# Kernel tuning notes

Measured on AMD Instinct MI355X. Metric: run time of the kernel, lower is better.

## Reference

```python
import jax, jax.numpy as jnp
import numpy as np

V, E, IN, OUT, K, NREL = 50000, 640000, 128, 128, 4, 237
D = IN // K   # 32
OD = OUT // K # 32

def setup_inputs() -> dict:
    key = jax.random.key(0)
    ks = jax.random.split(key, 20)
    s = 0.05
    return {
        'node_repr': jax.random.normal(ks[0], (V, IN), jnp.float32),
        'rel_repr': jax.random.normal(ks[1], (2 * NREL, IN), jnp.float32),
        'src': jax.random.randint(ks[2], (E,), 0, V, jnp.int32),
        'dst': jax.random.randint(ks[3], (E,), 0, V, jnp.int32),
        'etype': jax.random.randint(ks[4], (E,), 0, 2 * NREL, jnp.int32),
        'norm': jax.random.uniform(ks[5], (E,), jnp.float32),
        'node_w': jax.random.normal(ks[6], (K, IN, D), jnp.float32) * s,
        'node_rel_w': jax.random.normal(ks[7], (K, IN, D), jnp.float32) * s,
        'in_w': jax.random.normal(ks[8], (K, D, OD), jnp.float32) * s,
        'out_w': jax.random.normal(ks[9], (K, D, OD), jnp.float32) * s,
        'att_w': jax.random.normal(ks[10], (2 * D, 1), jnp.float32) * s,
        'loop_rel': jax.random.normal(ks[11], (1, IN), jnp.float32) * s,
        'loop_w': jax.random.normal(ks[12], (IN, OUT), jnp.float32) * s,
        'w_rel': jax.random.normal(ks[13], (IN, OUT), jnp.float32) * s,
        'bias': jnp.zeros((OUT,), jnp.float32),
        'bn_gamma': jnp.ones((OUT,), jnp.float32),
        'bn_beta': jnp.zeros((OUT,), jnp.float32),
    }

def reference(node_repr, rel_repr, src, dst, etype, norm,
              node_w, node_rel_w, in_w, out_w, att_w,
              loop_rel, loop_w, w_rel, bias, bn_gamma, bn_beta):
    e = E
    half = e // 2
    rel = rel_repr  # no bases
    # per-edge composition (opn='mult'): src feature * relation feature
    edge_comp = node_repr[src] * rel[etype]                      # [E, IN]
    edge_data = jnp.einsum('ei,kid->ekd', edge_comp, node_rel_w)  # [E, K, D]
    node_data = jnp.einsum('ei,kid->ekd', node_repr[dst], node_w) # [E, K, D]
    cat = jnp.concatenate([edge_data, node_data], axis=-1)       # [E, K, 2D]
    att = jax.nn.relu(cat @ att_w)                               # [E, K, 1]
    att = jax.nn.softmax(att, axis=1)                            # softmax over K factors
    edge_data = edge_data * att                                  # broadcast over D
    # factorized projection: first half edges -> in_w, second half -> out_w
    msg_in = jnp.einsum('ekd,kdo->eko', edge_data[:half], in_w)
    msg_out = jnp.einsum('ekd,kdo->eko', edge_data[half:], out_w)
    msg = jnp.concatenate([msg_in, msg_out], axis=0).reshape(e, OUT)
    msg = msg * norm[:, None]
    # scatter-sum into destination nodes, then /3 (drop_rate=0)
    h = jax.ops.segment_sum(msg, dst, num_segments=V) / 3.0      # [V, OUT]
    # self-loop term
    h = h + ((h * loop_rel) @ loop_w) / 3.0
    h = h + bias
    # BatchNorm1d (training-mode batch stats, biased variance, eps=1e-5)
    mean = jnp.mean(h, axis=0)
    var = jnp.var(h, axis=0)
    h = bn_gamma * (h - mean) * jax.lax.rsqrt(var + 1e-5) + bn_beta
    node_out = jnp.tanh(h)
    rel_out = rel @ w_rel
    return node_out, rel_out
```

## Files before the change

### kernel.cpp

```cpp
#include <hip/hip_runtime.h>

namespace {
constexpr int V = 50000;
constexpr int E = 640000;
constexpr int HALF = 320000;
constexpr int NREL2 = 474;
constexpr int C = 128;
constexpr int NCHUNK = (V + 255) / 256;
}

typedef _Float16 h4 __attribute__((ext_vector_type(4)));
typedef _Float16 f16x8 __attribute__((ext_vector_type(8)));
typedef float f32x4 __attribute__((ext_vector_type(4)));

__global__ void prep_kernel(const float* __restrict__ nrw, const float* __restrict__ nw,
                            const float* __restrict__ inw, const float* __restrict__ outw,
                            const float* __restrict__ aw,
                            float* __restrict__ cbuf, float* __restrict__ bbuf,
                            float* __restrict__ Min, float* __restrict__ Mout) {
  int tid = blockIdx.x * 256 + threadIdx.x;
  if (tid < 512) {
    int k = tid >> 7, i = tid & 127;
    float acc = 0.f;
    for (int d = 0; d < 32; ++d) acc += nrw[k*4096 + i*32 + d] * aw[d];
    cbuf[tid] = acc;
  } else if (tid < 1024) {
    int u = tid - 512; int k = u >> 7, i = u & 127;
    float acc = 0.f;
    for (int d = 0; d < 32; ++d) acc += nw[k*4096 + i*32 + d] * aw[32 + d];
    bbuf[u] = acc;
  } else if (tid < 1024 + 16384) {
    int u = tid - 1024; int k = u >> 12, rem = u & 4095, i = rem >> 5, o = rem & 31;
    float acc = 0.f;
    for (int d = 0; d < 32; ++d) acc += nrw[k*4096 + i*32 + d] * inw[k*1024 + d*32 + o];
    Min[u] = acc;
  } else if (tid < 1024 + 32768) {
    int u = tid - 1024 - 16384; int k = u >> 12, rem = u & 4095, i = rem >> 5, o = rem & 31;
    float acc = 0.f;
    for (int d = 0; d < 32; ++d) acc += nrw[k*4096 + i*32 + d] * outw[k*1024 + d*32 + o];
    Mout[u] = acc;
  }
}

__global__ void mh_kernel(const float* __restrict__ Min, const float* __restrict__ Mout,
                          _Float16* __restrict__ Mh) {
  int u = blockIdx.x * 256 + threadIdx.x;
  int i = u & 127;
  int o16 = (u >> 7) & 15;
  int ot = (u >> 11) & 1;
  int kk = (u >> 12) & 3;
  int d = (u >> 14) & 1;
  int o = ot * 16 + o16;
  float v = (d ? Mout : Min)[kk * 4096 + i * 32 + o];
  Mh[u] = (_Float16)v;
}

__global__ __launch_bounds__(256) void cast_kernel(const float* __restrict__ src,
                                                   _Float16* __restrict__ dst, int n8) {
  int u = blockIdx.x * 256 + threadIdx.x;
  if (u >= n8) return;
  const float4 v0 = *(const float4*)(src + (size_t)u * 8);
  const float4 v1 = *(const float4*)(src + (size_t)u * 8 + 4);
  f16x8 o;
  o[0] = (_Float16)v0.x; o[1] = (_Float16)v0.y;
  o[2] = (_Float16)v0.z; o[3] = (_Float16)v0.w;
  o[4] = (_Float16)v1.x; o[5] = (_Float16)v1.y;
  o[6] = (_Float16)v1.z; o[7] = (_Float16)v1.w;
  *(f16x8*)(dst + (size_t)u * 8) = o;
}

__global__ __launch_bounds__(256) void qnode_kernel(const float* __restrict__ nrp,
                                                    const float* __restrict__ bbuf,
                                                    float* __restrict__ qbuf) {
  const int t = blockIdx.x * 16 + (threadIdx.x >> 4);
  const int l = threadIdx.x & 15;
  if (t >= V) return;
  const float* row = nrp + (size_t)t * C + l * 8;
  float4 a0 = *(const float4*)(row);
  float4 a1 = *(const float4*)(row + 4);
  float p[4];
#pragma unroll
  for (int k = 0; k < 4; ++k) {
    const float* brow = bbuf + k * C + l * 8;
    float4 b0 = *(const float4*)(brow);
    float4 b1 = *(const float4*)(brow + 4);
    p[k] = a0.x * b0.x + a0.y * b0.y + a0.z * b0.z + a0.w * b0.w
         + a1.x * b1.x + a1.y * b1.y + a1.z * b1.z + a1.w * b1.w;
  }
#pragma unroll
  for (int m = 1; m < 16; m <<= 1) {
#pragma unroll
    for (int k = 0; k < 4; ++k) p[k] += __shfl_xor(p[k], m);
  }
  if (l == 0) *(float4*)(qbuf + 4 * (size_t)t) = make_float4(p[0], p[1], p[2], p[3]);
}

__global__ void hist_kernel(const int* __restrict__ dst, int* __restrict__ cnt,
                            int* __restrict__ cin) {
  int e = blockIdx.x * 256 + threadIdx.x;
  if (e < E) {
    int t = dst[e];
    atomicAdd(&cnt[t], 1);
    if (e < HALF) atomicAdd(&cin[t], 1);
  }
}

__global__ void scan_sum_kernel(const int* __restrict__ cnt, int* __restrict__ bsum) {
  __shared__ int sd[256];
  int tid = threadIdx.x;
  int idx = blockIdx.x * 256 + tid;
  int v = (idx < V) ? cnt[idx] : 0;
  sd[tid] = v; __syncthreads();
  for (int s = 128; s > 0; s >>= 1) {
    if (tid < s) sd[tid] += sd[tid + s];
    __syncthreads();
  }
  if (tid == 0) bsum[blockIdx.x] = sd[0];
}

__global__ void scan_top_kernel(int* __restrict__ bsum) {
  __shared__ int sd[256];
  int tid = threadIdx.x;
  int v = (tid < NCHUNK) ? bsum[tid] : 0;
  sd[tid] = v; __syncthreads();
  for (int ofs = 1; ofs < 256; ofs <<= 1) {
    int t = (tid >= ofs) ? sd[tid - ofs] : 0;
    __syncthreads();
    sd[tid] += t;
    __syncthreads();
  }
  if (tid < NCHUNK) bsum[tid] = sd[tid] - v;
}

__global__ void scan_apply_kernel(const int* __restrict__ cnt, const int* __restrict__ cin,
                                  const int* __restrict__ bsum, int4* __restrict__ ninfo) {
  __shared__ int sd[256];
  int tid = threadIdx.x;
  int idx = blockIdx.x * 256 + tid;
  int v = (idx < V) ? cnt[idx] : 0;
  sd[tid] = v; __syncthreads();
  for (int ofs = 1; ofs < 256; ofs <<= 1) {
    int t = (tid >= ofs) ? sd[tid - ofs] : 0;
    __syncthreads();
    sd[tid] += t;
    __syncthreads();
  }
  if (idx < V) {
    int off = bsum[blockIdx.x] + sd[tid] - v;
    ninfo[idx] = make_int4(off, v, cin[idx], 0);
  }
}

__global__ void place_kernel(const int* __restrict__ dst, const int* __restrict__ src,
                             const int* __restrict__ etype, const float* __restrict__ norm,
                             const int4* __restrict__ ninfo,
                             int* __restrict__ cur_in, int* __restrict__ cur_out,
                             int2* __restrict__ em) {
  int e = blockIdx.x * 256 + threadIdx.x;
  if (e < E) {
    int t = dst[e];
    int off = ninfo[t].x;
    int pos;
    if (e < HALF) {
      pos = off + atomicAdd(&cur_in[t], 1);
    } else {
      pos = off + ninfo[t].z + atomicAdd(&cur_out[t], 1);
    }
    em[pos] = make_int2(src[e] | (etype[e] << 16), __float_as_int(norm[e]));
  }
}

__global__ __launch_bounds__(256) void fused_kernel(
    const _Float16* __restrict__ nrp_h, const _Float16* __restrict__ rel_h,
    const int4* __restrict__ ninfo, const float* __restrict__ qbuf,
    const float* __restrict__ cbuf, const int2* __restrict__ em,
    const _Float16* __restrict__ Mh, float* __restrict__ h) {
  __shared__ __align__(16) _Float16 z16[16384];
  const int w = threadIdx.x >> 6;
  const int lane = threadIdx.x & 63;
  const int dirg = lane >> 5;
  const int slot = (lane >> 4) & 1;
  const int ll = lane & 15;
  const int ch0 = ll * 8;

  float4 ckA[4], ckB[4];
#pragma unroll
  for (int k = 0; k < 4; ++k) {
    ckA[k] = *(const float4*)(cbuf + k * C + ch0);
    ckB[k] = *(const float4*)(cbuf + k * C + ch0 + 4);
  }

  for (int nn = 0; nn < 4; ++nn) {
    const int node = w * 4 + nn;
    const int t = blockIdx.x * 16 + node;
    const int4 nfo = ninfo[t];
    const int start = nfo.x, deg = nfo.y, ni = nfo.z;
    const float4 q4 = *(const float4*)(qbuf + 4 * (size_t)t);
    const int sidx = dirg ? ni : 0;
    const int nmy = dirg ? (deg - ni) : ni;
    const int nmax = max(ni, deg - ni);

    float4 zA[4], zB[4];
#pragma unroll
    for (int k = 0; k < 4; ++k) {
      zA[k] = make_float4(0.f, 0.f, 0.f, 0.f);
      zB[k] = make_float4(0.f, 0.f, 0.f, 0.f);
    }

    if (nmax > 0) {
      int2 em0 = em[start + min(sidx + slot, deg - 1)];
      int2 em1 = em[start + min(sidx + 2 + slot, deg - 1)];
      f16x8 ah = *(const f16x8*)(nrp_h + (size_t)(em0.x & 0xFFFF) * C + ch0);
      f16x8 bh = *(const f16x8*)(rel_h + (size_t)((em0.x >> 16) & 0x1FF) * C + ch0);

      for (int j = 0; j < nmax; j += 2) {
        int2 em2 = em1;
        if (j + 4 < nmax) em2 = em[start + min(sidx + j + 4 + slot, deg - 1)];
        f16x8 ahn = ah, bhn = bh;
        if (j + 2 < nmax) {
          ahn = *(const f16x8*)(nrp_h + (size_t)(em1.x & 0xFFFF) * C + ch0);
          bhn = *(const f16x8*)(rel_h + (size_t)((em1.x >> 16) & 0x1FF) * C + ch0);
        }
        float4 xA, xB;
        xA.x = (float)ah[0] * (float)bh[0];
        xA.y = (float)ah[1] * (float)bh[1];
        xA.z = (float)ah[2] * (float)bh[2];
        xA.w = (float)ah[3] * (float)bh[3];
        xB.x = (float)ah[4] * (float)bh[4];
        xB.y = (float)ah[5] * (float)bh[5];
        xB.z = (float)ah[6] * (float)bh[6];
        xB.w = (float)ah[7] * (float)bh[7];
        float p0 = xA.x * ckA[0].x + xA.y * ckA[0].y + xA.z * ckA[0].z + xA.w * ckA[0].w
                 + xB.x * ckB[0].x + xB.y * ckB[0].y + xB.z * ckB[0].z + xB.w * ckB[0].w;
        float p1 = xA.x * ckA[1].x + xA.y * ckA[1].y + xA.z * ckA[1].z + xA.w * ckA[1].w
                 + xB.x * ckB[1].x + xB.y * ckB[1].y + xB.z * ckB[1].z + xB.w * ckB[1].w;
        float p2 = xA.x * ckA[2].x + xA.y * ckA[2].y + xA.z * ckA[2].z + xA.w * ckA[2].w
                 + xB.x * ckB[2].x + xB.y * ckB[2].y + xB.z * ckB[2].z + xB.w * ckB[2].w;
        float p3 = xA.x * ckA[3].x + xA.y * ckA[3].y + xA.z * ckA[3].z + xA.w * ckA[3].w
                 + xB.x * ckB[3].x + xB.y * ckB[3].y + xB.z * ckB[3].z + xB.w * ckB[3].w;
#pragma unroll
        for (int m = 1; m < 16; m <<= 1) {
          p0 += __shfl_xor(p0, m);
          p1 += __shfl_xor(p1, m);
          p2 += __shfl_xor(p2, m);
          p3 += __shfl_xor(p3, m);
        }
        float l0 = fmaxf(p0 + q4.x, 0.f);
        float l1 = fmaxf(p1 + q4.y, 0.f);
        float l2 = fmaxf(p2 + q4.z, 0.f);
        float l3 = fmaxf(p3 + q4.w, 0.f);
        float e0f = __expf(l0), e1f = __expf(l1);
        float e2f = __expf(l2), e3f = __expf(l3);
        float nr = __int_as_float(em0.y);
        float inv = ((j + slot) < nmy) ? (nr / (e0f + e1f + e2f + e3f)) : 0.f;
        float w0 = e0f * inv, w1 = e1f * inv, w2 = e2f * inv, w3 = e3f * inv;
        zA[0].x += w0 * xA.x; zA[0].y += w0 * xA.y; zA[0].z += w0 * xA.z; zA[0].w += w0 * xA.w;
        zB[0].x += w0 * xB.x; zB[0].y += w0 * xB.y; zB[0].z += w0 * xB.z; zB[0].w += w0 * xB.w;
        zA[1].x += w1 * xA.x; zA[1].y += w1 * xA.y; zA[1].z += w1 * xA.z; zA[1].w += w1 * xA.w;
        zB[1].x += w1 * xB.x; zB[1].y += w1 * xB.y; zB[1].z += w1 * xB.z; zB[1].w += w1 * xB.w;
        zA[2].x += w2 * xA.x; zA[2].y += w2 * xA.y; zA[2].z += w2 * xA.z; zA[2].w += w2 * xA.w;
        zB[2].x += w2 * xB.x; zB[2].y += w2 * xB.y; zB[2].z += w2 * xB.z; zB[2].w += w2 * xB.w;
        zA[3].x += w3 * xA.x; zA[3].y += w3 * xA.y; zA[3].z += w3 * xA.z; zA[3].w += w3 * xA.w;
        zB[3].x += w3 * xB.x; zB[3].y += w3 * xB.y; zB[3].z += w3 * xB.z; zB[3].w += w3 * xB.w;
        em0 = em1; em1 = em2;
        ah = ahn; bh = bhn;
      }
    }

#pragma unroll
    for (int k = 0; k < 4; ++k) {
      zA[k].x += __shfl_xor(zA[k].x, 16);
      zA[k].y += __shfl_xor(zA[k].y, 16);
      zA[k].z += __shfl_xor(zA[k].z, 16);
      zA[k].w += __shfl_xor(zA[k].w, 16);
      zB[k].x += __shfl_xor(zB[k].x, 16);
      zB[k].y += __shfl_xor(zB[k].y, 16);
      zB[k].z += __shfl_xor(zB[k].z, 16);
      zB[k].w += __shfl_xor(zB[k].w, 16);
    }
    if (slot == 0) {
      const int swz = (node & 7) << 4;
      char* zb = (char*)z16 + node * 2048 + dirg * 1024 + ((ll * 16) ^ swz);
#pragma unroll
      for (int k = 0; k < 4; ++k) {
        f16x8 o;
        o[0] = (_Float16)zA[k].x; o[1] = (_Float16)zA[k].y;
        o[2] = (_Float16)zA[k].z; o[3] = (_Float16)zA[k].w;
        o[4] = (_Float16)zB[k].x; o[5] = (_Float16)zB[k].y;
        o[6] = (_Float16)zB[k].z; o[7] = (_Float16)zB[k].w;
        *(f16x8*)(zb + k * 256) = o;
      }
    }
  }
  __syncthreads();

  const int kk = w;
  const int lo16 = lane & 15;
  const int kq = lane >> 4;
  {
    const int anode = lo16;
    const int aswz = (anode & 7) << 4;
    const char* zb = (const char*)z16 + anode * 2048 + kk * 256;
    f16x8 a[2][4];
#pragma unroll
    for (int d = 0; d < 2; ++d)
#pragma unroll
      for (int kc = 0; kc < 4; ++kc)
        a[d][kc] = *(const f16x8*)(zb + d * 1024 + ((kc * 64 + kq * 16) ^ aswz));

    f32x4 c0 = {0.f, 0.f, 0.f, 0.f};
    f32x4 c1 = {0.f, 0.f, 0.f, 0.f};
#pragma unroll
    for (int d = 0; d < 2; ++d)
#pragma unroll
      for (int kc = 0; kc < 4; ++kc) {
        const _Float16* mb = Mh + (((d * 4 + kk) * 2) * 16 + lo16) * 128 + kc * 32 + kq * 8;
        f16x8 b0 = *(const f16x8*)(mb);
        f16x8 b1 = *(const f16x8*)(mb + 2048);
        c0 = __builtin_amdgcn_mfma_f32_16x16x32_f16(a[d][kc], b0, c0, 0, 0, 0);
        c1 = __builtin_amdgcn_mfma_f32_16x16x32_f16(a[d][kc], b1, c1, 0, 0, 0);
      }

    const float third = 1.f / 3.f;
#pragma unroll
    for (int r = 0; r < 4; ++r) {
      int tt = blockIdx.x * 16 + kq * 4 + r;
      if (tt < V) {
        size_t hb = (size_t)tt * C + kk * 32 + lo16;
        h[hb] = c0[r] * third;
        h[hb + 16] = c1[r] * third;
      }
    }
  }
}

__global__ __launch_bounds__(256, 4) void selfloop_kernel(
    float* __restrict__ h, const float* __restrict__ lr,
    const float* __restrict__ lw, const float* __restrict__ bias,
    float* __restrict__ bnsum, float* __restrict__ bnsq) {
  __shared__ float xr[4][8][128];
  __shared__ float red[256];
  const int tid = threadIdx.x;
  const int w = tid >> 6, lane = tid & 63;

  const int c0 = 2 * lane, c1 = c0 + 1;
  const float lr0 = lr[c0], lr1 = lr[c1];
  const float bv0 = bias[c0], bv1 = bias[c1];
  float s0 = 0.f, s1 = 0.f, sq0 = 0.f, sq1 = 0.f;

  const int wg = blockIdx.x * 4 + w;
  const int nw = gridDim.x * 4;
  for (int rb = wg * 8; rb < V; rb += nw * 8) {
    const int nrows = min(8, V - rb);
    float2 hv[8];
#pragma unroll
    for (int rr = 0; rr < 8; ++rr) {
      if (rr < nrows) {
        hv[rr] = *(const float2*)(h + (size_t)(rb + rr) * C + c0);
      } else {
        hv[rr] = make_float2(0.f, 0.f);
      }
      xr[w][rr][c0] = hv[rr].x * lr0;
      xr[w][rr][c1] = hv[rr].y * lr1;
    }
    float acc[8][2] = {};
    for (int i = 0; i < C; ++i) {
      float2 lwv = *(const float2*)(lw + i * C + c0);
#pragma unroll
      for (int rr = 0; rr < 8; ++rr) {
        float xv = xr[w][rr][i];
        acc[rr][0] += xv * lwv.x;
        acc[rr][1] += xv * lwv.y;
      }
    }
    const float third = 1.f / 3.f;
#pragma unroll
    for (int rr = 0; rr < 8; ++rr) {
      if (rr < nrows) {
        float h0 = hv[rr].x + acc[rr][0] * third + bv0;
        float h1 = hv[rr].y + acc[rr][1] * third + bv1;
        *(float2*)(h + (size_t)(rb + rr) * C + c0) = make_float2(h0, h1);
        s0 += h0; s1 += h1; sq0 += h0 * h0; sq1 += h1 * h1;
      }
    }
  }

  __syncthreads();
  red[tid] = s0; __syncthreads();
  if (tid < 64) {
    float v = red[tid] + red[tid + 64] + red[tid + 128] + red[tid + 192];
    atomicAdd(&bnsum[2 * tid], v);
  }
  __syncthreads();
  red[tid] = s1; __syncthreads();
  if (tid < 64) {
    float v = red[tid] + red[tid + 64] + red[tid + 128] + red[tid + 192];
    atomicAdd(&bnsum[2 * tid + 1], v);
  }
  __syncthreads();
  red[tid] = sq0; __syncthreads();
  if (tid < 64) {
    float v = red[tid] + red[tid + 64] + red[tid + 128] + red[tid + 192];
    atomicAdd(&bnsq[2 * tid], v);
  }
  __syncthreads();
  red[tid] = sq1; __syncthreads();
  if (tid < 64) {
    float v = red[tid] + red[tid + 64] + red[tid + 128] + red[tid + 192];
    atomicAdd(&bnsq[2 * tid + 1], v);
  }
}

__global__ void tanh_kernel(float* __restrict__ h,
                            const float* __restrict__ bnsum, const float* __restrict__ bnsq,
                            const float* __restrict__ gamma, const float* __restrict__ beta) {
  int idx = blockIdx.x * 256 + threadIdx.x;
  int base = idx * 4;
  if (base >= V * C) return;
  int j = base & 127;
  const float invV = 1.f / (float)V;
  float4 v = *(float4*)(h + base);
  float o[4] = {v.x, v.y, v.z, v.w};
#pragma unroll
  for (int cidx = 0; cidx < 4; ++cidx) {
    float mean = bnsum[j + cidx] * invV;
    float var = bnsq[j + cidx] * invV - mean * mean;
    float sc = gamma[j + cidx] * rsqrtf(var + 1e-5f);
    float sh = beta[j + cidx] - sc * mean;
    o[cidx] = tanhf(sc * o[cidx] + sh);
  }
  v.x = o[0]; v.y = o[1]; v.z = o[2]; v.w = o[3];
  *(float4*)(h + base) = v;
}

__global__ __launch_bounds__(128) void relout_kernel(
    const float* __restrict__ rel, const float* __restrict__ wrel,
    float* __restrict__ out) {
  __shared__ float rr[128];
  int tid = threadIdx.x;
  int row = blockIdx.x;
  rr[tid] = rel[row * C + tid];
  __syncthreads();
  float acc = 0.f;
#pragma unroll 4
  for (int i = 0; i < C; ++i) acc += rr[i] * wrel[i * C + tid];
  out[row * C + tid] = acc;
}

extern "C" void kernel_launch(void* const* d_in, const int* in_sizes, int n_in,
                              void* d_out, int out_size, void* d_ws, size_t ws_size,
                              hipStream_t stream) {
  const float* node_repr  = (const float*)d_in[0];
  const float* rel_repr   = (const float*)d_in[1];
  const int*   src        = (const int*)d_in[2];
  const int*   dst        = (const int*)d_in[3];
  const int*   etype      = (const int*)d_in[4];
  const float* norm       = (const float*)d_in[5];
  const float* node_w     = (const float*)d_in[6];
  const float* node_rel_w = (const float*)d_in[7];
  const float* in_w       = (const float*)d_in[8];
  const float* out_w      = (const float*)d_in[9];
  const float* att_w      = (const float*)d_in[10];
  const float* loop_rel   = (const float*)d_in[11];
  const float* loop_w     = (const float*)d_in[12];
  const float* w_rel      = (const float*)d_in[13];
  const float* bias       = (const float*)d_in[14];
  const float* bn_gamma   = (const float*)d_in[15];
  const float* bn_beta    = (const float*)d_in[16];

  float* out = (float*)d_out;
  float* h = out;
  float* rel_out = out + (size_t)V * C;

  int* cnt = (int*)d_ws;
  int* cur_in = cnt + V;
  int* cin = cur_in + V;
  int* cur_out = cin + V;
  float* bnsum = (float*)(cur_out + V);
  float* bnsq = bnsum + 128;
  int* bsum = (int*)(bnsq + 128);
  int4* ninfo = (int4*)(bsum + 256);
  int2* em = (int2*)(ninfo + V);
  float* qbuf = (float*)(em + E);
  float* cbuf = qbuf + 4 * V;
  float* bbuf = cbuf + 512;
  float* Min = bbuf + 512;
  float* Mout = Min + 16384;
  _Float16* Mh = (_Float16*)(Mout + 16384);
  _Float16* nrp_h = Mh + 32768;
  _Float16* rel_h = nrp_h + (size_t)V * C;

  hipMemsetAsync(cnt, 0, (size_t)(4 * V + 256) * 4, stream);

  prep_kernel<<<(1024 + 32768 + 255) / 256, 256, 0, stream>>>(
      node_rel_w, node_w, in_w, out_w, att_w, cbuf, bbuf, Min, Mout);
  mh_kernel<<<128, 256, 0, stream>>>(Min, Mout, Mh);
  cast_kernel<<<(V * C / 8 + 255) / 256, 256, 0, stream>>>(node_repr, nrp_h, V * C / 8);
  cast_kernel<<<(NREL2 * C / 8 + 255) / 256, 256, 0, stream>>>(rel_repr, rel_h,
                                                               NREL2 * C / 8);
  qnode_kernel<<<(V + 15) / 16, 256, 0, stream>>>(node_repr, bbuf, qbuf);
  hist_kernel<<<E / 256, 256, 0, stream>>>(dst, cnt, cin);
  scan_sum_kernel<<<NCHUNK, 256, 0, stream>>>(cnt, bsum);
  scan_top_kernel<<<1, 256, 0, stream>>>(bsum);
  scan_apply_kernel<<<NCHUNK, 256, 0, stream>>>(cnt, cin, bsum, ninfo);
  place_kernel<<<E / 256, 256, 0, stream>>>(dst, src, etype, norm, ninfo,
                                            cur_in, cur_out, em);
  fused_kernel<<<(V + 15) / 16, 256, 0, stream>>>(nrp_h, rel_h, ninfo,
                                                  qbuf, cbuf, em, Mh, h);
  selfloop_kernel<<<1024, 256, 0, stream>>>(h, loop_rel, loop_w, bias, bnsum, bnsq);
  tanh_kernel<<<(V * C / 4 + 255) / 256, 256, 0, stream>>>(h, bnsum, bnsq, bn_gamma, bn_beta);
  relout_kernel<<<NREL2, 128, 0, stream>>>(rel_repr, w_rel, rel_out);
}
```

Before: 329.7 us.

## Fuse node fp16 cast into qnode, make fused kernel persistent, deepen prefetch

The fp16 cast of node features now happens inside qnode_kernel, which already reads each row, so one full pass over node_repr is removed. The fused edge-aggregation kernel becomes persistent with 1280 blocks looping over 16-node tiles, reusing per-block setup. The gather pipeline now prefetches node and relation rows two edge steps ahead instead of one, to hide gather latency. The costs are more registers per thread and coarser load balancing across blocks when node degrees vary.

```diff
diff --git a/kernel.cpp b/kernel.cpp
--- a/kernel.cpp
+++ b/kernel.cpp
@@ -7,6 +7,7 @@
 constexpr int NREL2 = 474;
 constexpr int C = 128;
 constexpr int NCHUNK = (V + 255) / 256;
+constexpr int NTILES = V / 16;
 }
 
 typedef _Float16 h4 __attribute__((ext_vector_type(4)));
@@ -71,13 +72,22 @@
 
 __global__ __launch_bounds__(256) void qnode_kernel(const float* __restrict__ nrp,
                                                     const float* __restrict__ bbuf,
-                                                    float* __restrict__ qbuf) {
+                                                    float* __restrict__ qbuf,
+                                                    _Float16* __restrict__ nrp_h) {
   const int t = blockIdx.x * 16 + (threadIdx.x >> 4);
   const int l = threadIdx.x & 15;
   if (t >= V) return;
   const float* row = nrp + (size_t)t * C + l * 8;
   float4 a0 = *(const float4*)(row);
   float4 a1 = *(const float4*)(row + 4);
+  {
+    f16x8 o;
+    o[0] = (_Float16)a0.x; o[1] = (_Float16)a0.y;
+    o[2] = (_Float16)a0.z; o[3] = (_Float16)a0.w;
+    o[4] = (_Float16)a1.x; o[5] = (_Float16)a1.y;
+    o[6] = (_Float16)a1.z; o[7] = (_Float16)a1.w;
+    *(f16x8*)(nrp_h + (size_t)t * C + l * 8) = o;
+  }
   float p[4];
 #pragma unroll
   for (int k = 0; k < 4; ++k) {
@@ -190,147 +200,151 @@
     ckB[k] = *(const float4*)(cbuf + k * C + ch0 + 4);
   }
 
-  for (int nn = 0; nn < 4; ++nn) {
-    const int node = w * 4 + nn;
-    const int t = blockIdx.x * 16 + node;
-    const int4 nfo = ninfo[t];
-    const int start = nfo.x, deg = nfo.y, ni = nfo.z;
-    const float4 q4 = *(const float4*)(qbuf + 4 * (size_t)t);
-    const int sidx = dirg ? ni : 0;
-    const int nmy = dirg ? (deg - ni) : ni;
-    const int nmax = max(ni, deg - ni);
-
-    float4 zA[4], zB[4];
-#pragma unroll
-    for (int k = 0; k < 4; ++k) {
-      zA[k] = make_float4(0.f, 0.f, 0.f, 0.f);
-      zB[k] = make_float4(0.f, 0.f, 0.f, 0.f);
+  for (int tile = blockIdx.x; tile < NTILES; tile += gridDim.x) {
+    for (int nn = 0; nn < 4; ++nn) {
+      const int node = w * 4 + nn;
+      const int t = tile * 16 + node;
+      const int4 nfo = ninfo[t];
+      const int start = nfo.x, deg = nfo.y, ni = nfo.z;
+      const float4 q4 = *(const float4*)(qbuf + 4 * (size_t)t);
+      const int sidx = dirg ? ni : 0;
+      const int nmy = dirg ? (deg - ni) : ni;
+      const int nmax = max(ni, deg - ni);
+
+      float4 zA[4], zB[4];
+#pragma unroll
+      for (int k = 0; k < 4; ++k) {
+        zA[k] = make_float4(0.f, 0.f, 0.f, 0.f);
+        zB[k] = make_float4(0.f, 0.f, 0.f, 0.f);
+      }
+
+      if (nmax > 0) {
+        int2 em0 = em[start + min(sidx + slot, deg - 1)];
+        int2 em1 = em[start + min(sidx + 2 + slot, deg - 1)];
+        int2 em2 = em[start + min(sidx + 4 + slot, deg - 1)];
+        f16x8 a0h = *(const f16x8*)(nrp_h + (size_t)(em0.x & 0xFFFF) * C + ch0);
+        f16x8 b0h = *(const f16x8*)(rel_h + (size_t)((em0.x >> 16) & 0x1FF) * C + ch0);
+        f16x8 a1h = *(const f16x8*)(nrp_h + (size_t)(em1.x & 0xFFFF) * C + ch0);
+        f16x8 b1h = *(const f16x8*)(rel_h + (size_t)((em1.x >> 16) & 0x1FF) * C + ch0);
+
+        for (int j = 0; j < nmax; j += 2) {
+          int2 em3 = em2;
+          if (j + 6 < nmax) em3 = em[start + min(sidx + j + 6 + slot, deg - 1)];
+          f16x8 a2h = a1h, b2h = b1h;
+          if (j + 4 < nmax) {
+            a2h = *(const f16x8*)(nrp_h + (size_t)(em2.x & 0xFFFF) * C + ch0);
+            b2h = *(const f16x8*)(rel_h + (size_t)((em2.x >> 16) & 0x1FF) * C + ch0);
+          }
+          float4 xA, xB;
+          xA.x = (float)a0h[0] * (float)b0h[0];
+          xA.y = (float)a0h[1] * (float)b0h[1];
+          xA.z = (float)a0h[2] * (float)b0h[2];
+          xA.w = (float)a0h[3] * (float)b0h[3];
+          xB.x = (float)a0h[4] * (float)b0h[4];
+          xB.y = (float)a0h[5] * (float)b0h[5];
+          xB.z = (float)a0h[6] * (float)b0h[6];
+          xB.w = (float)a0h[7] * (float)b0h[7];
+          float p0 = xA.x * ckA[0].x + xA.y * ckA[0].y + xA.z * ckA[0].z + xA.w * ckA[0].w
+                   + xB.x * ckB[0].x + xB.y * ckB[0].y + xB.z * ckB[0].z + xB.w * ckB[0].w;
+          float p1 = xA.x * ckA[1].x + xA.y * ckA[1].y + xA.z * ckA[1].z + xA.w * ckA[1].w
+                   + xB.x * ckB[1].x + xB.y * ckB[1].y + xB.z * ckB[1].z + xB.w * ckB[1].w;
+          float p2 = xA.x * ckA[2].x + xA.y * ckA[2].y + xA.z * ckA[2].z + xA.w * ckA[2].w
+                   + xB.x * ckB[2].x + xB.y * ckB[2].y + xB.z * ckB[2].z + xB.w * ckB[2].w;
+          float p3 = xA.x * ckA[3].x + xA.y * ckA[3].y + xA.z * ckA[3].z + xA.w * ckA[3].w
+                   + xB.x * ckB[3].x + xB.y * ckB[3].y + xB.z * ckB[3].z + xB.w * ckB[3].w;
+#pragma unroll
+          for (int m = 1; m < 16; m <<= 1) {
+            p0 += __shfl_xor(p0, m);
+            p1 += __shfl_xor(p1, m);
+            p2 += __shfl_xor(p2, m);
+            p3 += __shfl_xor(p3, m);
+          }
+          float l0 = fmaxf(p0 + q4.x, 0.f);
+          float l1 = fmaxf(p1 + q4.y, 0.f);
+          float l2 = fmaxf(p2 + q4.z, 0.f);
+          float l3 = fmaxf(p3 + q4.w, 0.f);
+          float e0f = __expf(l0), e1f = __expf(l1);
+          float e2f = __expf(l2), e3f = __expf(l3);
+          float nr = __int_as_float(em0.y);
+          float inv = ((j + slot) < nmy) ? (nr / (e0f + e1f + e2f + e3f)) : 0.f;
+          float w0 = e0f * inv, w1 = e1f * inv, w2 = e2f * inv, w3 = e3f * inv;
+          zA[0].x += w0 * xA.x; zA[0].y += w0 * xA.y; zA[0].z += w0 * xA.z; zA[0].w += w0 * xA.w;
+          zB[0].x += w0 * xB.x; zB[0].y += w0 * xB.y; zB[0].z += w0 * xB.z; zB[0].w += w0 * xB.w;
+          zA[1].x += w1 * xA.x; zA[1].y += w1 * xA.y; zA[1].z += w1 * xA.z; zA[1].w += w1 * xA.w;
+          zB[1].x += w1 * xB.x; zB[1].y += w1 * xB.y; zB[1].z += w1 * xB.z; zB[1].w += w1 * xB.w;
+          zA[2].x += w2 * xA.x; zA[2].y += w2 * xA.y; zA[2].z += w2 * xA.z; zA[2].w += w2 * xA.w;
+          zB[2].x += w2 * xB.x; zB[2].y += w2 * xB.y; zB[2].z += w2 * xB.z; zB[2].w += w2 * xB.w;
+          zA[3].x += w3 * xA.x; zA[3].y += w3 * xA.y; zA[3].z += w3 * xA.z; zA[3].w += w3 * xA.w;
+          zB[3].x += w3 * xB.x; zB[3].y += w3 * xB.y; zB[3].z += w3 * xB.z; zB[3].w += w3 * xB.w;
+          em0 = em1; em1 = em2; em2 = em3;
+          a0h = a1h; b0h = b1h; a1h = a2h; b1h = b2h;
+        }
+      }
+
+#pragma unroll
+      for (int k = 0; k < 4; ++k) {
+        zA[k].x += __shfl_xor(zA[k].x, 16);
+        zA[k].y += __shfl_xor(zA[k].y, 16);
+        zA[k].z += __shfl_xor(zA[k].z, 16);
+        zA[k].w += __shfl_xor(zA[k].w, 16);
+        zB[k].x += __shfl_xor(zB[k].x, 16);
+        zB[k].y += __shfl_xor(zB[k].y, 16);
+        zB[k].z += __shfl_xor(zB[k].z, 16);
+        zB[k].w += __shfl_xor(zB[k].w, 16);
+      }
+      if (slot == 0) {
+        const int swz = (node & 7) << 4;
+        char* zb = (char*)z16 + node * 2048 + dirg * 1024 + ((ll * 16) ^ swz);
+#pragma unroll
+        for (int k = 0; k < 4; ++k) {
+          f16x8 o;
+          o[0] = (_Float16)zA[k].x; o[1] = (_Float16)zA[k].y;
+          o[2] = (_Float16)zA[k].z; o[3] = (_Float16)zA[k].w;
+          o[4] = (_Float16)zB[k].x; o[5] = (_Float16)zB[k].y;
+          o[6] = (_Float16)zB[k].z; o[7] = (_Float16)zB[k].w;
+          *(f16x8*)(zb + k * 256) = o;
+        }
+      }
     }
-
-    if (nmax > 0) {
-      int2 em0 = em[start + min(sidx + slot, deg - 1)];
-      int2 em1 = em[start + min(sidx + 2 + slot, deg - 1)];
-      f16x8 ah = *(const f16x8*)(nrp_h + (size_t)(em0.x & 0xFFFF) * C + ch0);
-      f16x8 bh = *(const f16x8*)(rel_h + (size_t)((em0.x >> 16) & 0x1FF) * C + ch0);
-
-      for (int j = 0; j < nmax; j += 2) {
-        int2 em2 = em1;
-        if (j + 4 < nmax) em2 = em[start + min(sidx + j + 4 + slot, deg - 1)];
-        f16x8 ahn = ah, bhn = bh;
-        if (j + 2 < nmax) {
-          ahn = *(const f16x8*)(nrp_h + (size_t)(em1.x & 0xFFFF) * C + ch0);
-          bhn = *(const f16x8*)(rel_h + (size_t)((em1.x >> 16) & 0x1FF) * C + ch0);
+    __syncthreads();
+
+    {
+      const int kk = w;
+      const int lo16 = lane & 15;
+      const int kq = lane >> 4;
+      const int anode = lo16;
+      const int aswz = (anode & 7) << 4;
+      const char* zb = (const char*)z16 + anode * 2048 + kk * 256;
+      f16x8 a[2][4];
+#pragma unroll
+      for (int d = 0; d < 2; ++d)
+#pragma unroll
+        for (int kc = 0; kc < 4; ++kc)
+          a[d][kc] = *(const f16x8*)(zb + d * 1024 + ((kc * 64 + kq * 16) ^ aswz));
+
+      f32x4 c0 = {0.f, 0.f, 0.f, 0.f};
+      f32x4 c1 = {0.f, 0.f, 0.f, 0.f};
+#pragma unroll
+      for (int d = 0; d < 2; ++d)
+#pragma unroll
+        for (int kc = 0; kc < 4; ++kc) {
+          const _Float16* mb = Mh + (((d * 4 + kk) * 2) * 16 + lo16) * 128 + kc * 32 + kq * 8;
+          f16x8 b0 = *(const f16x8*)(mb);
+          f16x8 b1 = *(const f16x8*)(mb + 2048);
+          c0 = __builtin_amdgcn_mfma_f32_16x16x32_f16(a[d][kc], b0, c0, 0, 0, 0);
+          c1 = __builtin_amdgcn_mfma_f32_16x16x32_f16(a[d][kc], b1, c1, 0, 0, 0);
         }
-        float4 xA, xB;
-        xA.x = (float)ah[0] * (float)bh[0];
-        xA.y = (float)ah[1] * (float)bh[1];
-        xA.z = (float)ah[2] * (float)bh[2];
-        xA.w = (float)ah[3] * (float)bh[3];
-        xB.x = (float)ah[4] * (float)bh[4];
-        xB.y = (float)ah[5] * (float)bh[5];
-        xB.z = (float)ah[6] * (float)bh[6];
-        xB.w = (float)ah[7] * (float)bh[7];
-        float p0 = xA.x * ckA[0].x + xA.y * ckA[0].y + xA.z * ckA[0].z + xA.w * ckA[0].w
-                 + xB.x * ckB[0].x + xB.y * ckB[0].y + xB.z * ckB[0].z + xB.w * ckB[0].w;
-        float p1 = xA.x * ckA[1].x + xA.y * ckA[1].y + xA.z * ckA[1].z + xA.w * ckA[1].w
-                 + xB.x * ckB[1].x + xB.y * ckB[1].y + xB.z * ckB[1].z + xB.w * ckB[1].w;
-        float p2 = xA.x * ckA[2].x + xA.y * ckA[2].y + xA.z * ckA[2].z + xA.w * ckA[2].w
-                 + xB.x * ckB[2].x + xB.y * ckB[2].y + xB.z * ckB[2].z + xB.w * ckB[2].w;
-        float p3 = xA.x * ckA[3].x + xA.y * ckA[3].y + xA.z * ckA[3].z + xA.w * ckA[3].w
-                 + xB.x * ckB[3].x + xB.y * ckB[3].y + xB.z * ckB[3].z + xB.w * ckB[3].w;
-#pragma unroll
-        for (int m = 1; m < 16; m <<= 1) {
-          p0 += __shfl_xor(p0, m);
-          p1 += __shfl_xor(p1, m);
-          p2 += __shfl_xor(p2, m);
-          p3 += __shfl_xor(p3, m);
-        }
-        float l0 = fmaxf(p0 + q4.x, 0.f);
-        float l1 = fmaxf(p1 + q4.y, 0.f);
-        float l2 = fmaxf(p2 + q4.z, 0.f);
-        float l3 = fmaxf(p3 + q4.w, 0.f);
-        float e0f = __expf(l0), e1f = __expf(l1);
-        float e2f = __expf(l2), e3f = __expf(l3);
-        float nr = __int_as_float(em0.y);
-        float inv = ((j + slot) < nmy) ? (nr / (e0f + e1f + e2f + e3f)) : 0.f;
-        float w0 = e0f * inv, w1 = e1f * inv, w2 = e2f * inv, w3 = e3f * inv;
-        zA[0].x += w0 * xA.x; zA[0].y += w0 * xA.y; zA[0].z += w0 * xA.z; zA[0].w += w0 * xA.w;
-        zB[0].x += w0 * xB.x; zB[0].y += w0 * xB.y; zB[0].z += w0 * xB.z; zB[0].w += w0 * xB.w;
-        zA[1].x += w1 * xA.x; zA[1].y += w1 * xA.y; zA[1].z += w1 * xA.z; zA[1].w += w1 * xA.w;
-        zB[1].x += w1 * xB.x; zB[1].y += w1 * xB.y; zB[1].z += w1 * xB.z; zB[1].w += w1 * xB.w;
-        zA[2].x += w2 * xA.x; zA[2].y += w2 * xA.y; zA[2].z += w2 * xA.z; zA[2].w += w2 * xA.w;
-        zB[2].x += w2 * xB.x; zB[2].y += w2 * xB.y; zB[2].z += w2 * xB.z; zB[2].w += w2 * xB.w;
-        zA[3].x += w3 * xA.x; zA[3].y += w3 * xA.y; zA[3].z += w3 * xA.z; zA[3].w += w3 * xA.w;
-        zB[3].x += w3 * xB.x; zB[3].y += w3 * xB.y; zB[3].z += w3 * xB.z; zB[3].w += w3 * xB.w;
-        em0 = em1; em1 = em2;
-        ah = ahn; bh = bhn;
-      }
-    }
-
-#pragma unroll
-    for (int k = 0; k < 4; ++k) {
-      zA[k].x += __shfl_xor(zA[k].x, 16);
-      zA[k].y += __shfl_xor(zA[k].y, 16);
-      zA[k].z += __shfl_xor(zA[k].z, 16);
-      zA[k].w += __shfl_xor(zA[k].w, 16);
-      zB[k].x += __shfl_xor(zB[k].x, 16);
-      zB[k].y += __shfl_xor(zB[k].y, 16);
-      zB[k].z += __shfl_xor(zB[k].z, 16);
-      zB[k].w += __shfl_xor(zB[k].w, 16);
-    }
-    if (slot == 0) {
-      const int swz = (node & 7) << 4;
-      char* zb = (char*)z16 + node * 2048 + dirg * 1024 + ((ll * 16) ^ swz);
-#pragma unroll
-      for (int k = 0; k < 4; ++k) {
-        f16x8 o;
-        o[0] = (_Float16)zA[k].x; o[1] = (_Float16)zA[k].y;
-        o[2] = (_Float16)zA[k].z; o[3] = (_Float16)zA[k].w;
-        o[4] = (_Float16)zB[k].x; o[5] = (_Float16)zB[k].y;
-        o[6] = (_Float16)zB[k].z; o[7] = (_Float16)zB[k].w;
-        *(f16x8*)(zb + k * 256) = o;
-      }
-    }
-  }
-  __syncthreads();
-
-  const int kk = w;
-  const int lo16 = lane & 15;
-  const int kq = lane >> 4;
-  {
-    const int anode = lo16;
-    const int aswz = (anode & 7) << 4;
-    const char* zb = (const char*)z16 + anode * 2048 + kk * 256;
-    f16x8 a[2][4];
-#pragma unroll
-    for (int d = 0; d < 2; ++d)
-#pragma unroll
-      for (int kc = 0; kc < 4; ++kc)
-        a[d][kc] = *(const f16x8*)(zb + d * 1024 + ((kc * 64 + kq * 16) ^ aswz));
-
-    f32x4 c0 = {0.f, 0.f, 0.f, 0.f};
-    f32x4 c1 = {0.f, 0.f, 0.f, 0.f};
-#pragma unroll
-    for (int d = 0; d < 2; ++d)
-#pragma unroll
-      for (int kc = 0; kc < 4; ++kc) {
-        const _Float16* mb = Mh + (((d * 4 + kk) * 2) * 16 + lo16) * 128 + kc * 32 + kq * 8;
-        f16x8 b0 = *(const f16x8*)(mb);
-        f16x8 b1 = *(const f16x8*)(mb + 2048);
-        c0 = __builtin_amdgcn_mfma_f32_16x16x32_f16(a[d][kc], b0, c0, 0, 0, 0);
-        c1 = __builtin_amdgcn_mfma_f32_16x16x32_f16(a[d][kc], b1, c1, 0, 0, 0);
-      }
-
-    const float third = 1.f / 3.f;
-#pragma unroll
-    for (int r = 0; r < 4; ++r) {
-      int tt = blockIdx.x * 16 + kq * 4 + r;
-      if (tt < V) {
+
+      const float third = 1.f / 3.f;
+#pragma unroll
+      for (int r = 0; r < 4; ++r) {
+        int tt = tile * 16 + kq * 4 + r;
         size_t hb = (size_t)tt * C + kk * 32 + lo16;
         h[hb] = c0[r] * third;
         h[hb + 16] = c1[r] * third;
       }
     }
+    __syncthreads();
   }
 }
 
@@ -495,18 +509,17 @@
   prep_kernel<<<(1024 + 32768 + 255) / 256, 256, 0, stream>>>(
       node_rel_w, node_w, in_w, out_w, att_w, cbuf, bbuf, Min, Mout);
   mh_kernel<<<128, 256, 0, stream>>>(Min, Mout, Mh);
-  cast_kernel<<<(V * C / 8 + 255) / 256, 256, 0, stream>>>(node_repr, nrp_h, V * C / 8);
   cast_kernel<<<(NREL2 * C / 8 + 255) / 256, 256, 0, stream>>>(rel_repr, rel_h,
                                                                NREL2 * C / 8);
-  qnode_kernel<<<(V + 15) / 16, 256, 0, stream>>>(node_repr, bbuf, qbuf);
+  qnode_kernel<<<(V + 15) / 16, 256, 0, stream>>>(node_repr, bbuf, qbuf, nrp_h);
   hist_kernel<<<E / 256, 256, 0, stream>>>(dst, cnt, cin);
   scan_sum_kernel<<<NCHUNK, 256, 0, stream>>>(cnt, bsum);
   scan_top_kernel<<<1, 256, 0, stream>>>(bsum);
   scan_apply_kernel<<<NCHUNK, 256, 0, stream>>>(cnt, cin, bsum, ninfo);
   place_kernel<<<E / 256, 256, 0, stream>>>(dst, src, etype, norm, ninfo,
                                             cur_in, cur_out, em);
-  fused_kernel<<<(V + 15) / 16, 256, 0, stream>>>(nrp_h, rel_h, ninfo,
-                                                  qbuf, cbuf, em, Mh, h);
+  fused_kernel<<<1280, 256, 0, stream>>>(nrp_h, rel_h, ninfo, qbuf, cbuf, em,
+                                         Mh, h);
   selfloop_kernel<<<1024, 256, 0, stream>>>(h, loop_rel, loop_w, bias, bnsum, bnsq);
   tanh_kernel<<<(V * C / 4 + 255) / 256, 256, 0, stream>>>(h, bnsum, bnsq, bn_gamma, bn_beta);
   relout_kernel<<<NREL2, 128, 0, stream>>>(rel_repr, w_rel, rel_out);
```

New measurement: 353.3 us. 1.07x slower.
